# Kernel optimization log

Hardware: AMD Instinct MI355X
Metric: run time of the kernel (lower is better)

Reference implementation:

```python
import jax, jax.numpy as jnp
import numpy as np

LOG1000 = 6.9077542789816375  # ln(1000)


def setup_inputs() -> dict:
    key = jax.random.key(0)
    kx, kp = jax.random.split(key)
    x = jax.random.normal(kx, (65536, 128), dtype=jnp.float32)
    points = jax.random.normal(kp, (2048, 128), dtype=jnp.float32)
    beta_raw = jnp.array([-3.5], dtype=jnp.float32)
    return {"x": x, "points": points, "beta_raw": beta_raw}


def reference(x, points, beta_raw):
    t1 = jnp.sum(x * x, axis=-1, keepdims=True)            # [N, 1]
    t2 = jnp.sum(points * points, axis=-1)[None, :]        # [1, P]
    t3 = 2.0 * jnp.einsum('nd,pd->np', x, points)          # [N, P]
    d2 = jnp.clip(t1 + t2 - t3, 0.0)
    min_d = jnp.min(d2, axis=-1)                           # [N]
    # translated sigmoid
    beta = jax.nn.softplus(beta_raw)                       # [1]
    alpha = -beta * LOG1000
    return jax.nn.sigmoid((min_d + alpha) / beta)
```

## Files before the change

### kernel.cpp

```cpp
#include <hip/hip_runtime.h>


#define NROWS 65536
#define NPTS  2048
#define DIMS  128
#define LOG1000F 6.9077542789816375f
#define STAGE_PTS 256
#define NSTAGES (NPTS / STAGE_PTS)

typedef __attribute__((ext_vector_type(8))) int i32x8;
typedef __attribute__((ext_vector_type(4))) float f32x4;

union AFrag { int d[8]; i32x8 v; };
union BFrag { uint4 u4[2]; i32x8 v; };

__global__ __launch_bounds__(256) void prep_points_kernel(
    const float* __restrict__ pts, unsigned char* __restrict__ ptsf8,
    float* __restrict__ pnorm)
{
    int tid  = threadIdx.x;
    int lane = tid & 63;
    int w    = tid >> 6;
    int pt   = blockIdx.x * 4 + w;
    const float2 v = *reinterpret_cast<const float2*>(
        pts + (size_t)pt * DIMS + lane * 2);
    int pk = __builtin_amdgcn_cvt_pk_fp8_f32(v.x, v.y, 0, false);
    *reinterpret_cast<unsigned short*>(ptsf8 + (size_t)pt * DIMS + lane * 2) =
        (unsigned short)(pk & 0xFFFF);
    float ss = v.x * v.x + v.y * v.y;
    ss += __shfl_xor(ss, 1, 64);
    ss += __shfl_xor(ss, 2, 64);
    ss += __shfl_xor(ss, 4, 64);
    ss += __shfl_xor(ss, 8, 64);
    ss += __shfl_xor(ss, 16, 64);
    ss += __shfl_xor(ss, 32, 64);
    if (lane == 0) pnorm[pt] = ss;
}

__global__ __launch_bounds__(256, 2) void distnet_main_kernel(
    const float* __restrict__ x, const unsigned char* __restrict__ ptsf8,
    const float* __restrict__ pnorm, const float* __restrict__ beta_raw,
    float* __restrict__ out)
{
    __shared__ uint4 s_b[2][STAGE_PTS * DIMS / 16];
    __shared__ float s_pn[NPTS];
    __shared__ float s_xn[128];

    int tid  = threadIdx.x;
    for (int i = tid; i < NPTS / 4; i += 256)
        *reinterpret_cast<float4*>(&s_pn[i * 4]) =
            reinterpret_cast<const float4*>(pnorm)[i];

    int wave = tid >> 6;
    int lane = tid & 63;
    int m    = lane & 15;
    int q    = lane >> 4;
    int r0   = blockIdx.x * 128 + wave * 32;

    AFrag afrag[2];
#pragma unroll
    for (int t = 0; t < 2; ++t) {
        const float* xp = x + (size_t)(r0 + t * 16 + m) * DIMS + q * 32;
        float ss = 0.f;
#pragma unroll
        for (int d = 0; d < 8; ++d) {
            float4 v = *reinterpret_cast<const float4*>(xp + d * 4);
            int w0 = __builtin_amdgcn_cvt_pk_fp8_f32(v.x, v.y, 0, false);
            w0 = __builtin_amdgcn_cvt_pk_fp8_f32(v.z, v.w, w0, true);
            afrag[t].d[d] = w0;
            ss += v.x * v.x + v.y * v.y + v.z * v.z + v.w * v.w;
        }
        ss += __shfl_xor(ss, 16, 64);
        ss += __shfl_xor(ss, 32, 64);
        if (lane < 16) s_xn[wave * 32 + t * 16 + lane] = ss;
    }

    const unsigned char* gbase = ptsf8;
    auto issue_stage = [&](int s, int buf) {
#pragma unroll
        for (int i = 0; i < 8; ++i) {
            int tt = wave * 4 + (i >> 1);
            int c  = i & 1;
            size_t pbyte = (size_t)(s * STAGE_PTS + tt * 16 + m) * DIMS
                           + (size_t)q * 32 + (size_t)c * 16;
            const void* g = gbase + pbyte;
            void* l = (void*)&s_b[buf][(tt * 2 + c) * 64];
            __builtin_amdgcn_global_load_lds(
                (const __attribute__((address_space(1))) unsigned int*)g,
                (__attribute__((address_space(3))) unsigned int*)l,
                16, 0, 0);
        }
    };

    issue_stage(0, 0);

    float runmin[2][4] = {{1e30f, 1e30f, 1e30f, 1e30f},
                          {1e30f, 1e30f, 1e30f, 1e30f}};

    for (int s = 0; s < NSTAGES; ++s) {
        __syncthreads();
        if (s + 1 < NSTAGES) issue_stage(s + 1, (s + 1) & 1);

        const uint4* bbuf = &s_b[s & 1][0];
#pragma unroll
        for (int t = 0; t < 16; ++t) {
            BFrag bf;
            bf.u4[0] = bbuf[(t * 2 + 0) * 64 + lane];
            bf.u4[1] = bbuf[(t * 2 + 1) * 64 + lane];
            float pn = s_pn[s * STAGE_PTS + t * 16 + m];
            f32x4 acc0 = {0.f, 0.f, 0.f, 0.f};
            f32x4 acc1 = {0.f, 0.f, 0.f, 0.f};
            acc0 = __builtin_amdgcn_mfma_scale_f32_16x16x128_f8f6f4(
                afrag[0].v, bf.v, acc0, 0, 0, 0, 0x7F7F7F7F, 0, 0x7F7F7F7F);
            acc1 = __builtin_amdgcn_mfma_scale_f32_16x16x128_f8f6f4(
                afrag[1].v, bf.v, acc1, 0, 0, 0, 0x7F7F7F7F, 0, 0x7F7F7F7F);
#pragma unroll
            for (int r = 0; r < 4; ++r) {
                runmin[0][r] = fminf(runmin[0][r], fmaf(-2.f, acc0[r], pn));
                runmin[1][r] = fminf(runmin[1][r], fmaf(-2.f, acc1[r], pn));
            }
        }
    }

    float br    = beta_raw[0];
    float beta  = log1pf(expf(br));
    float alpha = -beta * LOG1000F;
#pragma unroll
    for (int t = 0; t < 2; ++t) {
#pragma unroll
        for (int r = 0; r < 4; ++r) {
            float v = runmin[t][r];
            v = fminf(v, __shfl_xor(v, 1, 64));
            v = fminf(v, __shfl_xor(v, 2, 64));
            v = fminf(v, __shfl_xor(v, 4, 64));
            v = fminf(v, __shfl_xor(v, 8, 64));
            if (m == 0) {
                float xnv = s_xn[wave * 32 + t * 16 + q * 4 + r];
                float d2  = fmaxf(xnv + v, 0.f);
                float z   = (d2 + alpha) / beta;
                out[r0 + t * 16 + q * 4 + r] = 1.f / (1.f + expf(-z));
            }
        }
    }
}

extern "C" void kernel_launch(void* const* d_in, const int* in_sizes, int n_in,
                              void* d_out, int out_size, void* d_ws, size_t ws_size,
                              hipStream_t stream) {
    const float* x        = (const float*)d_in[0];
    const float* pts      = (const float*)d_in[1];
    const float* beta_raw = (const float*)d_in[2];
    float* out            = (float*)d_out;

    unsigned char* ptsf8 = (unsigned char*)d_ws;
    float* pnorm = (float*)((char*)d_ws + (size_t)NPTS * DIMS);

    prep_points_kernel<<<NPTS / 4, 256, 0, stream>>>(pts, ptsf8, pnorm);
    distnet_main_kernel<<<NROWS / 128, 256, 0, stream>>>(x, ptsf8, pnorm,
                                                         beta_raw, out);
}
```

Baseline: 100.6 us.

## Pre-swizzle fp8 points into fragment layout and stream B directly from global

The prep kernel now writes fp8 points in the exact MFMA B-fragment order, so the main kernel reads fragments straight from global/L2 with a 4-deep register pipeline instead of staging through LDS with per-stage barriers. Each wave pair covers 64 rows (4 A fragments per wave), and the two waves split the 2048 points in half, combining their partial maxima through shared memory. The -0.5*||p||^2 term is folded into the accumulator init so the min becomes a max with no extra FMA per element. This removes LDS traffic and syncs and raises A reuse per B load, but depends on L2 bandwidth and latency hiding for the direct global fragment loads.

```diff
diff --git a/kernel.cpp b/kernel.cpp
--- a/kernel.cpp
+++ b/kernel.cpp
@@ -5,8 +5,6 @@
 #define NPTS  2048
 #define DIMS  128
 #define LOG1000F 6.9077542789816375f
-#define STAGE_PTS 256
-#define NSTAGES (NPTS / STAGE_PTS)
 
 typedef __attribute__((ext_vector_type(8))) int i32x8;
 typedef __attribute__((ext_vector_type(4))) float f32x4;
@@ -25,7 +23,12 @@
     const float2 v = *reinterpret_cast<const float2*>(
         pts + (size_t)pt * DIMS + lane * 2);
     int pk = __builtin_amdgcn_cvt_pk_fp8_f32(v.x, v.y, 0, false);
-    *reinterpret_cast<unsigned short*>(ptsf8 + (size_t)pt * DIMS + lane * 2) =
+    int T  = pt >> 4, pm = pt & 15;
+    int q  = lane >> 4;
+    int c  = (lane >> 3) & 1;
+    int j  = (lane & 7) * 2;
+    size_t dst = (size_t)((T * 2 + c) * 64 + q * 16 + pm) * 16 + j;
+    *reinterpret_cast<unsigned short*>(ptsf8 + dst) =
         (unsigned short)(pk & 0xFFFF);
     float ss = v.x * v.x + v.y * v.y;
     ss += __shfl_xor(ss, 1, 64);
@@ -42,105 +45,110 @@
     const float* __restrict__ pnorm, const float* __restrict__ beta_raw,
     float* __restrict__ out)
 {
-    __shared__ uint4 s_b[2][STAGE_PTS * DIMS / 16];
-    __shared__ float s_pn[NPTS];
+    __shared__ __align__(16) float s_pn[NPTS];
+    __shared__ float s_red[2][128];
     __shared__ float s_xn[128];
 
-    int tid  = threadIdx.x;
-    for (int i = tid; i < NPTS / 4; i += 256)
-        *reinterpret_cast<float4*>(&s_pn[i * 4]) =
-            reinterpret_cast<const float4*>(pnorm)[i];
+    int tid = threadIdx.x;
+    {
+        const float4* p4 = reinterpret_cast<const float4*>(pnorm);
+        float4* d4 = reinterpret_cast<float4*>(s_pn);
+        float4 a = p4[tid], b = p4[tid + 256];
+        d4[tid]       = make_float4(-.5f*a.x, -.5f*a.y, -.5f*a.z, -.5f*a.w);
+        d4[tid + 256] = make_float4(-.5f*b.x, -.5f*b.y, -.5f*b.z, -.5f*b.w);
+    }
 
-    int wave = tid >> 6;
-    int lane = tid & 63;
-    int m    = lane & 15;
-    int q    = lane >> 4;
-    int r0   = blockIdx.x * 128 + wave * 32;
+    int wid   = tid >> 6, lane = tid & 63;
+    int m     = lane & 15, q = lane >> 4;
+    int pairw = wid >> 1, half = wid & 1;
+    int rbase = blockIdx.x * 128 + pairw * 64;
 
-    AFrag afrag[2];
+    AFrag afrag[4];
 #pragma unroll
-    for (int t = 0; t < 2; ++t) {
-        const float* xp = x + (size_t)(r0 + t * 16 + m) * DIMS + q * 32;
-        float ss = 0.f;
+    for (int t = 0; t < 4; ++t) {
+        const float* xp = x + (size_t)(rbase + t * 16 + m) * DIMS + q * 32;
+        float s = 0.f;
 #pragma unroll
         for (int d = 0; d < 8; ++d) {
             float4 v = *reinterpret_cast<const float4*>(xp + d * 4);
             int w0 = __builtin_amdgcn_cvt_pk_fp8_f32(v.x, v.y, 0, false);
             w0 = __builtin_amdgcn_cvt_pk_fp8_f32(v.z, v.w, w0, true);
             afrag[t].d[d] = w0;
-            ss += v.x * v.x + v.y * v.y + v.z * v.z + v.w * v.w;
+            s += v.x * v.x + v.y * v.y + v.z * v.z + v.w * v.w;
         }
-        ss += __shfl_xor(ss, 16, 64);
-        ss += __shfl_xor(ss, 32, 64);
-        if (lane < 16) s_xn[wave * 32 + t * 16 + lane] = ss;
+        s += __shfl_xor(s, 16, 64);
+        s += __shfl_xor(s, 32, 64);
+        if (half == 0 && q == 0) s_xn[pairw * 64 + t * 16 + m] = s;
     }
+    __syncthreads();
 
-    const unsigned char* gbase = ptsf8;
-    auto issue_stage = [&](int s, int buf) {
+    float runmax[4][4];
 #pragma unroll
-        for (int i = 0; i < 8; ++i) {
-            int tt = wave * 4 + (i >> 1);
-            int c  = i & 1;
-            size_t pbyte = (size_t)(s * STAGE_PTS + tt * 16 + m) * DIMS
-                           + (size_t)q * 32 + (size_t)c * 16;
-            const void* g = gbase + pbyte;
-            void* l = (void*)&s_b[buf][(tt * 2 + c) * 64];
-            __builtin_amdgcn_global_load_lds(
-                (const __attribute__((address_space(1))) unsigned int*)g,
-                (__attribute__((address_space(3))) unsigned int*)l,
-                16, 0, 0);
+    for (int t = 0; t < 4; ++t)
+#pragma unroll
+        for (int r = 0; r < 4; ++r) runmax[t][r] = -1e30f;
+
+    const uint4* bsw = reinterpret_cast<const uint4*>(ptsf8);
+    const int T0 = half * 64;
+
+    BFrag bA, bB, bC, bD;
+    float pnA, pnB, pnC, pnD;
+
+#define LOADT(gT, buf, pnh) do {                       \
+        buf.u4[0] = bsw[(gT) * 128 + lane];            \
+        buf.u4[1] = bsw[(gT) * 128 + 64 + lane];       \
+        pnh = s_pn[(gT) * 16 + m];                     \
+    } while (0)
+
+    auto compute = [&](const BFrag& buf, float pnh) {
+#pragma unroll
+        for (int t = 0; t < 4; ++t) {
+            f32x4 acc = {pnh, pnh, pnh, pnh};
+            acc = __builtin_amdgcn_mfma_scale_f32_16x16x128_f8f6f4(
+                afrag[t].v, buf.v, acc, 0, 0, 0, 0x7F7F7F7F, 0, 0x7F7F7F7F);
+#pragma unroll
+            for (int r = 0; r < 4; ++r)
+                runmax[t][r] = fmaxf(runmax[t][r], acc[r]);
         }
     };
 
-    issue_stage(0, 0);
+    LOADT(T0 + 0, bA, pnA);
+    LOADT(T0 + 1, bB, pnB);
+    for (int T = 0; T < 64; T += 4) {
+        LOADT(T0 + T + 2, bC, pnC);
+        compute(bA, pnA);
+        LOADT(T0 + T + 3, bD, pnD);
+        compute(bB, pnB);
+        if (T + 4 < 64) LOADT(T0 + T + 4, bA, pnA);
+        compute(bC, pnC);
+        if (T + 5 < 64) LOADT(T0 + T + 5, bB, pnB);
+        compute(bD, pnD);
+    }
+#undef LOADT
 
-    float runmin[2][4] = {{1e30f, 1e30f, 1e30f, 1e30f},
-                          {1e30f, 1e30f, 1e30f, 1e30f}};
-
-    for (int s = 0; s < NSTAGES; ++s) {
-        __syncthreads();
-        if (s + 1 < NSTAGES) issue_stage(s + 1, (s + 1) & 1);
-
-        const uint4* bbuf = &s_b[s & 1][0];
 #pragma unroll
-        for (int t = 0; t < 16; ++t) {
-            BFrag bf;
-            bf.u4[0] = bbuf[(t * 2 + 0) * 64 + lane];
-            bf.u4[1] = bbuf[(t * 2 + 1) * 64 + lane];
-            float pn = s_pn[s * STAGE_PTS + t * 16 + m];
-            f32x4 acc0 = {0.f, 0.f, 0.f, 0.f};
-            f32x4 acc1 = {0.f, 0.f, 0.f, 0.f};
-            acc0 = __builtin_amdgcn_mfma_scale_f32_16x16x128_f8f6f4(
-                afrag[0].v, bf.v, acc0, 0, 0, 0, 0x7F7F7F7F, 0, 0x7F7F7F7F);
-            acc1 = __builtin_amdgcn_mfma_scale_f32_16x16x128_f8f6f4(
-                afrag[1].v, bf.v, acc1, 0, 0, 0, 0x7F7F7F7F, 0, 0x7F7F7F7F);
+    for (int t = 0; t < 4; ++t) {
 #pragma unroll
-            for (int r = 0; r < 4; ++r) {
-                runmin[0][r] = fminf(runmin[0][r], fmaf(-2.f, acc0[r], pn));
-                runmin[1][r] = fminf(runmin[1][r], fmaf(-2.f, acc1[r], pn));
-            }
+        for (int r = 0; r < 4; ++r) {
+            float v = runmax[t][r];
+            v = fmaxf(v, __shfl_xor(v, 1, 64));
+            v = fmaxf(v, __shfl_xor(v, 2, 64));
+            v = fmaxf(v, __shfl_xor(v, 4, 64));
+            v = fmaxf(v, __shfl_xor(v, 8, 64));
+            if (m == 0)
+                s_red[half][pairw * 64 + t * 16 + q * 4 + r] = v;
         }
     }
+    __syncthreads();
 
-    float br    = beta_raw[0];
-    float beta  = log1pf(expf(br));
-    float alpha = -beta * LOG1000F;
-#pragma unroll
-    for (int t = 0; t < 2; ++t) {
-#pragma unroll
-        for (int r = 0; r < 4; ++r) {
-            float v = runmin[t][r];
-            v = fminf(v, __shfl_xor(v, 1, 64));
-            v = fminf(v, __shfl_xor(v, 2, 64));
-            v = fminf(v, __shfl_xor(v, 4, 64));
-            v = fminf(v, __shfl_xor(v, 8, 64));
-            if (m == 0) {
-                float xnv = s_xn[wave * 32 + t * 16 + q * 4 + r];
-                float d2  = fmaxf(xnv + v, 0.f);
-                float z   = (d2 + alpha) / beta;
-                out[r0 + t * 16 + q * 4 + r] = 1.f / (1.f + expf(-z));
-            }
-        }
+    if (tid < 128) {
+        float vmax  = fmaxf(s_red[0][tid], s_red[1][tid]);
+        float d2    = fmaxf(fmaf(-2.f, vmax, s_xn[tid]), 0.f);
+        float br    = beta_raw[0];
+        float beta  = log1pf(expf(br));
+        float alpha = -beta * LOG1000F;
+        float z     = (d2 + alpha) / beta;
+        out[(size_t)blockIdx.x * 128 + tid] = 1.f / (1.f + expf(-z));
     }
 }
 
```

New measurement: 95.49 us. 5.1% less time.
